# Kernel optimization log

Measured on AMD Instinct MI355X. Metric: run time of the kernel, lower is better.

Reference implementation:

```python
import jax, jax.numpy as jnp
import numpy as np

B, N, A, O = 16, 128, 32, 64
VD, QD, H = 768, 768, 1024


def setup_inputs() -> dict:
    key = jax.random.key(0)
    ks = jax.random.split(key, 10)
    inp = {
        "q": jax.random.normal(ks[0], (B, N, 1, QD), dtype=jnp.float32),
        "att1": jax.random.uniform(ks[1], (B, N, A, O), dtype=jnp.float32),
        "obj_reps": jax.random.normal(ks[2], (B, O, VD), dtype=jnp.float32),
        "tags_attention": jax.random.randint(ks[3], (B, N, A), 0, 2, dtype=jnp.int32),
        "t": 1,
        # FCNet (weight_norm Linear + ReLU) params; dropout is identity at eval
        "vw": jax.random.normal(ks[4], (H, VD), dtype=jnp.float32) * (1.0 / np.sqrt(VD)),
        "vb": jnp.zeros((H,), dtype=jnp.float32),
        "qw": jax.random.normal(ks[5], (H, QD), dtype=jnp.float32) * (1.0 / np.sqrt(QD)),
        "qb": jnp.zeros((H,), dtype=jnp.float32),
        "lw": jax.random.normal(ks[6], (1, H), dtype=jnp.float32) * (1.0 / np.sqrt(H)),
        "lb": jnp.zeros((1,), dtype=jnp.float32),
    }
    return inp


def reference(q, att1, obj_reps, tags_attention, t, vw, vb, qw, qb, lw, lb):
    # v: [b,n,a,d] = att1 [b,n,a,o] contracted with obj_reps [b,o,d]
    v = jnp.einsum('bnao,bod->bnad', att1, obj_reps)
    # FCNet projections (weight_norm linear + ReLU, dropout off at eval)
    v_proj = jax.nn.relu(jnp.einsum('bnad,hd->bnah', v, vw) + vb)      # [b,n,a,h]
    q_proj = jax.nn.relu(jnp.einsum('bnkd,hd->bnkh', q, qw) + qb)      # [b,n,1,h]
    joint = v_proj * q_proj                                            # broadcast over a
    logits = (jnp.einsum('bnah,oh->bnao', joint, lw) + lb)[..., 0]     # [b,n,a]
    logits = logits / jnp.asarray(t, logits.dtype)
    mask = (tags_attention > 0)
    masked_logits = jnp.where(mask, logits, jnp.asarray(-1e30, logits.dtype))
    att2 = jax.nn.softmax(masked_logits, axis=-1)                       # [b,n,a]
    # att2[:,:,None,:] @ att1 -> [b,n,1,o] -> squeeze
    attention_last = jnp.einsum('bna,bnao->bno', att2, att1)
    return attention_last
```

## Files before the change

kernel.cpp:

```cpp
#include <hip/hip_runtime.h>

#define B_ 16
#define N_ 128
#define A_ 32
#define O_ 64
#define VD_ 768
#define H_ 1024

typedef short s16x8 __attribute__((ext_vector_type(8)));
typedef short s16x4 __attribute__((ext_vector_type(4)));
typedef float f32x4 __attribute__((ext_vector_type(4)));

#define MFMA(a, b, c) __builtin_amdgcn_mfma_f32_16x16x32_bf16(a, b, c, 0, 0, 0)

__device__ __forceinline__ short bf_hi(float x) {
    return (short)(__float_as_uint(x) >> 16);
}
__device__ __forceinline__ short bf_lo(float x) {
    float r = x - __uint_as_float(__float_as_uint(x) & 0xffff0000u);
    return (short)(__float_as_uint(r) >> 16);
}

__device__ __forceinline__ void gload16(const void* g, void* l) {
    __builtin_amdgcn_global_load_lds(
        (const __attribute__((address_space(1))) void*)g,
        (__attribute__((address_space(3))) void*)l, 16, 0, 0);
}

__global__ __launch_bounds__(256)
void cvt_split(const float* __restrict__ obj, const float* __restrict__ q,
               const float* __restrict__ vw, const float* __restrict__ qw,
               short* __restrict__ objh, short* __restrict__ objl,
               short* __restrict__ qh, short* __restrict__ ql,
               short* __restrict__ vwh, short* __restrict__ qwh)
{
    const int bid = blockIdx.x;
    const float* src; short* hi; short* lo; int base4;
    if (bid < 192)      { src = obj; hi = objh; lo = objl; base4 = bid * 1024; }
    else if (bid < 576) { src = q;   hi = qh;   lo = ql;   base4 = (bid - 192) * 1024; }
    else if (bid < 768) { src = vw;  hi = vwh;  lo = nullptr; base4 = (bid - 576) * 1024; }
    else                { src = qw;  hi = qwh;  lo = nullptr; base4 = (bid - 768) * 1024; }
    #pragma unroll
    for (int it = 0; it < 4; ++it) {
        const size_t f4 = (size_t)base4 + it * 256 + threadIdx.x;
        const float4 v = *(const float4*)(src + f4 * 4);
        const float ff[4] = {v.x, v.y, v.z, v.w};
        s16x4 h4;
        #pragma unroll
        for (int e = 0; e < 4; ++e) h4[e] = bf_hi(ff[e]);
        *(s16x4*)(hi + f4 * 4) = h4;
        if (lo) {
            s16x4 l4;
            #pragma unroll
            for (int e = 0; e < 4; ++e) l4[e] = bf_lo(ff[e]);
            *(s16x4*)(lo + f4 * 4) = l4;
        }
    }
}

__global__ __launch_bounds__(256)
void gemm_split(const short* __restrict__ objh, const short* __restrict__ objl,
                const short* __restrict__ qh, const short* __restrict__ ql,
                const short* __restrict__ vwh, const short* __restrict__ qwh,
                const float* __restrict__ qb, const float* __restrict__ lwp,
                short* __restrict__ Wth, float* __restrict__ ub)
{
    __shared__ __align__(16) short lds[3 * 4096];
    const int bid = blockIdx.x;
    const bool isA = bid < 256;
    const int lb_ = isA ? bid : bid - 256;
    const int r0 = (lb_ >> 4) * 64;
    const int h0 = (lb_ & 15) * 64;
    const short* Xh = isA ? objh : qh;
    const short* Xl = isA ? objl : ql;
    const short* Bh = isA ? vwh : qwh;

    const int tid = threadIdx.x;
    const int w = tid >> 6, l = tid & 63;
    const int wm = (w >> 1) * 32, wn = (w & 1) * 32;
    const int g = l >> 4, c16 = l & 15;

    const int row0 = tid >> 3, u0 = (tid & 7) ^ (row0 & 7);
    const int unit1 = 256 + tid;
    const int row1 = unit1 >> 3, u1 = (unit1 & 7) ^ (row1 & 7);
    const short* pXh = Xh + (size_t)r0 * VD_;
    const short* pXl = Xl + (size_t)r0 * VD_;
    const short* pBh = Bh + (size_t)h0 * VD_;
    int go0 = row0 * VD_ + u0 * 8;
    int go1 = row1 * VD_ + u1 * 8;
    short* const d0 = &lds[w * 512];

    f32x4 acc[2][2] = {};

    for (int c = 0; c < VD_ / 64; ++c) {
        __syncthreads();
        gload16(pXh + go0, d0);
        gload16(pXh + go1, d0 + 2048);
        gload16(pXl + go0, d0 + 4096);
        gload16(pXl + go1, d0 + 4096 + 2048);
        gload16(pBh + go0, d0 + 8192);
        gload16(pBh + go1, d0 + 8192 + 2048);
        go0 += 64; go1 += 64;
        __syncthreads();
        #pragma unroll
        for (int s = 0; s < 2; ++s) {
            s16x8 ah[2], al[2], bh2[2];
            #pragma unroll
            for (int i = 0; i < 2; ++i) {
                const int m = wm + i * 16 + c16;
                const int us = (((s * 4 + g) ^ (m & 7)) * 8);
                ah[i]  = *(const s16x8*)&lds[m * 64 + us];
                al[i]  = *(const s16x8*)&lds[4096 + m * 64 + us];
                const int n = wn + i * 16 + c16;
                const int vs = (((s * 4 + g) ^ (n & 7)) * 8);
                bh2[i] = *(const s16x8*)&lds[8192 + n * 64 + vs];
            }
            #pragma unroll
            for (int i = 0; i < 2; ++i)
                #pragma unroll
                for (int j = 0; j < 2; ++j) {
                    acc[i][j] = MFMA(ah[i], bh2[j], acc[i][j]);
                    acc[i][j] = MFMA(al[i], bh2[j], acc[i][j]);
                }
        }
    }

    #pragma unroll
    for (int i = 0; i < 2; ++i)
        #pragma unroll
        for (int j = 0; j < 2; ++j) {
            const int h = h0 + wn + j * 16 + c16;
            if (isA) {
                const int o = wm + i * 16 + g * 4;
                s16x4 hi4;
                #pragma unroll
                for (int r = 0; r < 4; ++r) hi4[r] = bf_hi(acc[i][j][r]);
                const size_t dst = ((size_t)(lb_ >> 4) * H_ + h) * O_ + o;
                *(s16x4*)&Wth[dst] = hi4;
            } else {
                const float bv = qb[h], sv = lwp[h];
                #pragma unroll
                for (int r = 0; r < 4; ++r) {
                    const int m = r0 + wm + i * 16 + g * 4 + r;
                    ub[(size_t)m * H_ + h] = fmaxf(acc[i][j][r] + bv, 0.f) * sv;
                }
            }
        }
}

__global__ __launch_bounds__(256, 4)
void fused_logits(const float* __restrict__ att1, const short* __restrict__ Wth,
                  const float* __restrict__ ub, const float* __restrict__ vb,
                  const int* __restrict__ tags, const int* __restrict__ tptr,
                  const float* __restrict__ lbptr, float* __restrict__ out)
{
    __shared__ __align__(16) short Ah[64 * 64];
    __shared__ __align__(16) short Wc[2][4096];
    __shared__ float ut[2][1024];
    __shared__ float vbl[1024];
    __shared__ float lgp[4][64];

    const int blk = blockIdx.x;
    const int b = blk >> 6;
    const int n0 = (blk & 63) * 2;
    const int tid = threadIdx.x;
    const size_t base_row = (size_t)(b * N_ + n0) * A_;

    const int w = tid >> 6, l = tid & 63;
    const int g = l >> 4, c16 = l & 15;

    const int r0l = l >> 3;
    const int cu  = (l & 7) ^ r0l;
    const short* pW = Wth + (size_t)b * (H_ * O_) + w * 1024 + r0l * 64 + cu * 8;
    short* const dW = &Wc[0][w * 1024 + l * 8];

#define STAGEW(BUFOFF, CI) do { \
        const short* ph_ = pW + (size_t)(CI) * 4096; \
        gload16(ph_,       dW + (BUFOFF)); \
        gload16(ph_ + 512, dW + (BUFOFF) + 512); \
    } while (0)

    STAGEW(0, 0);

    {
        const int row = tid >> 2, qq = tid & 3;
        const float* src = att1 + (base_row + row) * O_ + qq * 16;
        #pragma unroll
        for (int uu = 0; uu < 2; ++uu) {
            const float4 f0 = *(const float4*)(src + uu * 8);
            const float4 f1 = *(const float4*)(src + uu * 8 + 4);
            const float ff[8] = {f0.x, f0.y, f0.z, f0.w, f1.x, f1.y, f1.z, f1.w};
            const int us = ((qq * 2 + uu) ^ (row & 7)) * 8;
            s16x8 hi;
            #pragma unroll
            for (int e = 0; e < 8; ++e) hi[e] = bf_hi(ff[e]);
            *(s16x8*)&Ah[row * 64 + us] = hi;
        }
    }

    {
        const float* u0g = ub + (size_t)(b * N_ + n0) * H_;
        const float* u1g = u0g + H_;
        *(float4*)&ut[0][tid * 4] = *(const float4*)(u0g + tid * 4);
        *(float4*)&ut[1][tid * 4] = *(const float4*)(u1g + tid * 4);
        *(float4*)&vbl[tid * 4]   = *(const float4*)(vb + tid * 4);
    }

    __syncthreads();

    s16x8 ahf[4][2];
    #pragma unroll
    for (int i = 0; i < 4; ++i)
        #pragma unroll
        for (int s = 0; s < 2; ++s) {
            const int m = i * 16 + c16;
            const int us = ((s * 4 + g) ^ (m & 7)) * 8;
            ahf[i][s] = *(const s16x8*)&Ah[m * 64 + us];
        }

    const int sr = c16 & 7;
    const int rb = w * 1024 + c16 * 64;
    const int ubo0 = (g ^ sr) * 8;
    const int ubo1 = ((g + 4) ^ sr) * 8;
    const int ulane = w * 16 + c16;

    f32x4 part[4] = {};

    #pragma unroll 2
    for (int t = 0; t < 16; ++t) {
        if (t < 15) {
            STAGEW(((t + 1) & 1) * 4096, t + 1);
            asm volatile("s_waitcnt vmcnt(2)" ::: "memory");
        } else {
            asm volatile("s_waitcnt vmcnt(0)" ::: "memory");
        }
        const int bufo = (t & 1) * 4096;
        const float vbv = vbl[t * 64 + ulane];
        const float uu0 = ut[0][t * 64 + ulane];
        const float uu1 = ut[1][t * 64 + ulane];
        const s16x8 bh0 = *(const s16x8*)&Wc[0][bufo + rb + ubo0];
        const s16x8 bh1 = *(const s16x8*)&Wc[0][bufo + rb + ubo1];
        #pragma unroll
        for (int i = 0; i < 4; ++i) {
            f32x4 acc = {};
            acc = MFMA(ahf[i][0], bh0, acc);
            acc = MFMA(ahf[i][1], bh1, acc);
            const float uu = (i < 2) ? uu0 : uu1;
            #pragma unroll
            for (int r = 0; r < 4; ++r)
                part[i][r] += fmaxf(acc[r] + vbv, 0.f) * uu;
        }
    }
#undef STAGEW

    __syncthreads();

    #pragma unroll
    for (int i = 0; i < 4; ++i)
        #pragma unroll
        for (int r = 0; r < 4; ++r) {
            float v = part[i][r];
            v += __shfl_xor(v, 1, 64);
            v += __shfl_xor(v, 2, 64);
            v += __shfl_xor(v, 4, 64);
            v += __shfl_xor(v, 8, 64);
            if (c16 == 0) lgp[w][i * 16 + g * 4 + r] = v;
        }
    __syncthreads();

    float* sml = &vbl[0];
    if (tid < 64) {
        const float tf = (float)(*tptr);
        const float lsum = lgp[0][tid] + lgp[1][tid] + lgp[2][tid] + lgp[3][tid];
        const float lv = (lsum + *lbptr) / tf;
        const int tg = tags[base_row + tid];
        sml[tid] = (tg > 0) ? lv : -1e30f;
    }
    __syncthreads();

    if (tid < 128) {
        const int nn = tid >> 6, o = tid & 63;
        const float* lr = &sml[nn * 32];
        float m = -3.0e38f;
        #pragma unroll
        for (int a = 0; a < 32; ++a) m = fmaxf(m, lr[a]);
        float s = 0.f, accum = 0.f;
        #pragma unroll
        for (int a = 0; a < 32; ++a) {
            const float e = __expf(lr[a] - m);
            s += e;
            accum += e * att1[(base_row + nn * 32 + a) * O_ + o];
        }
        out[(size_t)(b * N_ + n0 + nn) * O_ + o] = accum / s;
    }
}

extern "C" void kernel_launch(void* const* d_in, const int* in_sizes, int n_in,
                              void* d_out, int out_size, void* d_ws, size_t ws_size,
                              hipStream_t stream)
{
    const float* q    = (const float*)d_in[0];
    const float* att1 = (const float*)d_in[1];
    const float* obj  = (const float*)d_in[2];
    const int*   tags = (const int*)d_in[3];
    const int*   tptr = (const int*)d_in[4];
    const float* vw   = (const float*)d_in[5];
    const float* vb   = (const float*)d_in[6];
    const float* qw   = (const float*)d_in[7];
    const float* qb   = (const float*)d_in[8];
    const float* lw   = (const float*)d_in[9];
    const float* lb   = (const float*)d_in[10];
    float* out = (float*)d_out;

    float* ub   = (float*)d_ws;
    short* Wth  = (short*)(ub + (size_t)B_ * N_ * H_);
    short* objh = Wth + (size_t)B_ * H_ * O_;
    short* objl = objh + (size_t)1024 * VD_;
    short* qh   = objl + (size_t)1024 * VD_;
    short* ql   = qh + (size_t)2048 * VD_;
    short* vwh  = ql + (size_t)2048 * VD_;
    short* qwh  = vwh + (size_t)H_ * VD_;

    cvt_split<<<960, 256, 0, stream>>>(obj, q, vw, qw, objh, objl, qh, ql,
                                       vwh, qwh);
    gemm_split<<<768, 256, 0, stream>>>(objh, objl, qh, ql, vwh, qwh,
                                        qb, lw, Wth, ub);
    fused_logits<<<B_ * 64, 256, 0, stream>>>(att1, Wth, ub, vb, tags,
                                              tptr, lb, out);
}
```

Measured before the change: 48.30 us.

## Double-buffer gemm_split LDS loads and drop low-part split for obj GEMM

Replaces the single-buffered load/compute loop in gemm_split with a two-stage LDS double buffer driven by manual vmcnt waits and raw barriers, so global-to-LDS loads for chunk c+2 overlap MFMA work on chunk c. The obj-side GEMM also stops using the bf16 low-part correction: the objl conversion, its loads and the second MFMA per tile are removed for those blocks. This cuts conversion traffic, load traffic and MFMA count. The cost is lower precision on the Wth path and reliance on hand-counted vmcnt values that must match the number of issued loads per stage.

```diff
diff --git a/kernel.cpp b/kernel.cpp
--- a/kernel.cpp
+++ b/kernel.cpp
@@ -30,14 +30,14 @@
 __global__ __launch_bounds__(256)
 void cvt_split(const float* __restrict__ obj, const float* __restrict__ q,
                const float* __restrict__ vw, const float* __restrict__ qw,
-               short* __restrict__ objh, short* __restrict__ objl,
+               short* __restrict__ objh,
                short* __restrict__ qh, short* __restrict__ ql,
                short* __restrict__ vwh, short* __restrict__ qwh)
 {
     const int bid = blockIdx.x;
     const float* src; short* hi; short* lo; int base4;
-    if (bid < 192)      { src = obj; hi = objh; lo = objl; base4 = bid * 1024; }
-    else if (bid < 576) { src = q;   hi = qh;   lo = ql;   base4 = (bid - 192) * 1024; }
+    if (bid < 192)      { src = obj; hi = objh; lo = nullptr; base4 = bid * 1024; }
+    else if (bid < 576) { src = q;   hi = qh;   lo = ql;      base4 = (bid - 192) * 1024; }
     else if (bid < 768) { src = vw;  hi = vwh;  lo = nullptr; base4 = (bid - 576) * 1024; }
     else                { src = qw;  hi = qwh;  lo = nullptr; base4 = (bid - 768) * 1024; }
     #pragma unroll
@@ -59,20 +59,20 @@
 }
 
 __global__ __launch_bounds__(256)
-void gemm_split(const short* __restrict__ objh, const short* __restrict__ objl,
+void gemm_split(const short* __restrict__ objh,
                 const short* __restrict__ qh, const short* __restrict__ ql,
                 const short* __restrict__ vwh, const short* __restrict__ qwh,
                 const float* __restrict__ qb, const float* __restrict__ lwp,
                 short* __restrict__ Wth, float* __restrict__ ub)
 {
-    __shared__ __align__(16) short lds[3 * 4096];
+    __shared__ __align__(16) short lds[2][3][4096];
     const int bid = blockIdx.x;
     const bool isA = bid < 256;
     const int lb_ = isA ? bid : bid - 256;
     const int r0 = (lb_ >> 4) * 64;
     const int h0 = (lb_ & 15) * 64;
     const short* Xh = isA ? objh : qh;
-    const short* Xl = isA ? objl : ql;
+    const short* Xl = ql;
     const short* Bh = isA ? vwh : qwh;
 
     const int tid = threadIdx.x;
@@ -86,22 +86,40 @@
     const short* pXh = Xh + (size_t)r0 * VD_;
     const short* pXl = Xl + (size_t)r0 * VD_;
     const short* pBh = Bh + (size_t)h0 * VD_;
-    int go0 = row0 * VD_ + u0 * 8;
-    int go1 = row1 * VD_ + u1 * 8;
-    short* const d0 = &lds[w * 512];
+    const int go0 = row0 * VD_ + u0 * 8;
+    const int go1 = row1 * VD_ + u1 * 8;
+    const int wo = w * 512;
+
+#define STAGE(BUF, CI) do { \
+        const int co_ = (CI) * 64; \
+        gload16(pXh + go0 + co_, &lds[BUF][0][wo]); \
+        gload16(pXh + go1 + co_, &lds[BUF][0][wo + 2048]); \
+        if (!isA) { \
+            gload16(pXl + go0 + co_, &lds[BUF][1][wo]); \
+            gload16(pXl + go1 + co_, &lds[BUF][1][wo + 2048]); \
+        } \
+        gload16(pBh + go0 + co_, &lds[BUF][2][wo]); \
+        gload16(pBh + go1 + co_, &lds[BUF][2][wo + 2048]); \
+    } while (0)
+
+    STAGE(0, 0);
+    STAGE(1, 1);
 
     f32x4 acc[2][2] = {};
 
+    #pragma unroll 2
     for (int c = 0; c < VD_ / 64; ++c) {
-        __syncthreads();
-        gload16(pXh + go0, d0);
-        gload16(pXh + go1, d0 + 2048);
-        gload16(pXl + go0, d0 + 4096);
-        gload16(pXl + go1, d0 + 4096 + 2048);
-        gload16(pBh + go0, d0 + 8192);
-        gload16(pBh + go1, d0 + 8192 + 2048);
-        go0 += 64; go1 += 64;
-        __syncthreads();
+        if (c < VD_ / 64 - 1) {
+            if (isA) asm volatile("s_waitcnt vmcnt(4)" ::: "memory");
+            else     asm volatile("s_waitcnt vmcnt(6)" ::: "memory");
+        } else {
+            asm volatile("s_waitcnt vmcnt(0)" ::: "memory");
+        }
+        asm volatile("s_barrier" ::: "memory");
+
+        const short* bXh = &lds[c & 1][0][0];
+        const short* bXl = &lds[c & 1][1][0];
+        const short* bBh = &lds[c & 1][2][0];
         #pragma unroll
         for (int s = 0; s < 2; ++s) {
             s16x8 ah[2], al[2], bh2[2];
@@ -109,21 +127,27 @@
             for (int i = 0; i < 2; ++i) {
                 const int m = wm + i * 16 + c16;
                 const int us = (((s * 4 + g) ^ (m & 7)) * 8);
-                ah[i]  = *(const s16x8*)&lds[m * 64 + us];
-                al[i]  = *(const s16x8*)&lds[4096 + m * 64 + us];
+                ah[i]  = *(const s16x8*)&bXh[m * 64 + us];
+                if (!isA) al[i] = *(const s16x8*)&bXl[m * 64 + us];
                 const int n = wn + i * 16 + c16;
                 const int vs = (((s * 4 + g) ^ (n & 7)) * 8);
-                bh2[i] = *(const s16x8*)&lds[8192 + n * 64 + vs];
+                bh2[i] = *(const s16x8*)&bBh[n * 64 + vs];
             }
             #pragma unroll
             for (int i = 0; i < 2; ++i)
                 #pragma unroll
                 for (int j = 0; j < 2; ++j) {
                     acc[i][j] = MFMA(ah[i], bh2[j], acc[i][j]);
-                    acc[i][j] = MFMA(al[i], bh2[j], acc[i][j]);
+                    if (!isA) acc[i][j] = MFMA(al[i], bh2[j], acc[i][j]);
                 }
         }
-    }
+
+        asm volatile("s_waitcnt lgkmcnt(0)" ::: "memory");
+        __builtin_amdgcn_sched_barrier(0);
+        asm volatile("s_barrier" ::: "memory");
+        if (c + 2 < VD_ / 64) STAGE(c & 1, c + 2);
+    }
+#undef STAGE
 
     #pragma unroll
     for (int i = 0; i < 2; ++i)
@@ -315,15 +339,13 @@
     float* ub   = (float*)d_ws;
     short* Wth  = (short*)(ub + (size_t)B_ * N_ * H_);
     short* objh = Wth + (size_t)B_ * H_ * O_;
-    short* objl = objh + (size_t)1024 * VD_;
-    short* qh   = objl + (size_t)1024 * VD_;
+    short* qh   = objh + (size_t)1024 * VD_;
     short* ql   = qh + (size_t)2048 * VD_;
     short* vwh  = ql + (size_t)2048 * VD_;
     short* qwh  = vwh + (size_t)H_ * VD_;
 
-    cvt_split<<<960, 256, 0, stream>>>(obj, q, vw, qw, objh, objl, qh, ql,
-                                       vwh, qwh);
-    gemm_split<<<768, 256, 0, stream>>>(objh, objl, qh, ql, vwh, qwh,
+    cvt_split<<<960, 256, 0, stream>>>(obj, q, vw, qw, objh, qh, ql, vwh, qwh);
+    gemm_split<<<768, 256, 0, stream>>>(objh, qh, ql, vwh, qwh,
                                         qb, lw, Wth, ub);
     fused_logits<<<B_ * 64, 256, 0, stream>>>(att1, Wth, ub, vb, tags,
                                               tptr, lb, out);
```

Result: faster. 46.29 us (-4.2%).

## Fuse bf16 conversion into GEMM with register-prefetched double-buffered LDS

Applied to the files above, without the earlier changes.

Removes the separate conversion kernel and has the GEMM load fp32 inputs directly, truncate them to bf16 in registers, and write into a double-buffered LDS tile. The next-next chunk is prefetched into registers while the current one is computed. It also drops the hi/lo split on the activations, which halves the MFMA count but lowers the precision of the obj/q projections to plain bf16. One kernel launch and the intermediate bf16 global round-trip go away, at the cost of more register pressure and synchronous global loads inside the loop.

```diff
diff --git a/kernel.cpp b/kernel.cpp
--- a/kernel.cpp
+++ b/kernel.cpp
@@ -16,9 +16,11 @@
 __device__ __forceinline__ short bf_hi(float x) {
     return (short)(__float_as_uint(x) >> 16);
 }
-__device__ __forceinline__ short bf_lo(float x) {
-    float r = x - __uint_as_float(__float_as_uint(x) & 0xffff0000u);
-    return (short)(__float_as_uint(r) >> 16);
+__device__ __forceinline__ void cvthi8(const float4& f0, const float4& f1,
+                                       s16x8& hi) {
+    const float ff[8] = {f0.x, f0.y, f0.z, f0.w, f1.x, f1.y, f1.z, f1.w};
+    #pragma unroll
+    for (int e = 0; e < 8; ++e) hi[e] = bf_hi(ff[e]);
 }
 
 __device__ __forceinline__ void gload16(const void* g, void* l) {
@@ -27,103 +29,93 @@
         (__attribute__((address_space(3))) void*)l, 16, 0, 0);
 }
 
-__global__ __launch_bounds__(256)
-void cvt_split(const float* __restrict__ obj, const float* __restrict__ q,
-               const float* __restrict__ vw, const float* __restrict__ qw,
-               short* __restrict__ objh, short* __restrict__ objl,
-               short* __restrict__ qh, short* __restrict__ ql,
-               short* __restrict__ vwh, short* __restrict__ qwh)
+__global__ __launch_bounds__(256, 3)
+void gemm_cvt(const float* __restrict__ obj, const float* __restrict__ q,
+              const float* __restrict__ vw, const float* __restrict__ qw,
+              const float* __restrict__ qb, const float* __restrict__ lwp,
+              short* __restrict__ Wth, float* __restrict__ ub)
 {
-    const int bid = blockIdx.x;
-    const float* src; short* hi; short* lo; int base4;
-    if (bid < 192)      { src = obj; hi = objh; lo = objl; base4 = bid * 1024; }
-    else if (bid < 576) { src = q;   hi = qh;   lo = ql;   base4 = (bid - 192) * 1024; }
-    else if (bid < 768) { src = vw;  hi = vwh;  lo = nullptr; base4 = (bid - 576) * 1024; }
-    else                { src = qw;  hi = qwh;  lo = nullptr; base4 = (bid - 768) * 1024; }
-    #pragma unroll
-    for (int it = 0; it < 4; ++it) {
-        const size_t f4 = (size_t)base4 + it * 256 + threadIdx.x;
-        const float4 v = *(const float4*)(src + f4 * 4);
-        const float ff[4] = {v.x, v.y, v.z, v.w};
-        s16x4 h4;
-        #pragma unroll
-        for (int e = 0; e < 4; ++e) h4[e] = bf_hi(ff[e]);
-        *(s16x4*)(hi + f4 * 4) = h4;
-        if (lo) {
-            s16x4 l4;
-            #pragma unroll
-            for (int e = 0; e < 4; ++e) l4[e] = bf_lo(ff[e]);
-            *(s16x4*)(lo + f4 * 4) = l4;
-        }
-    }
-}
-
-__global__ __launch_bounds__(256)
-void gemm_split(const short* __restrict__ objh, const short* __restrict__ objl,
-                const short* __restrict__ qh, const short* __restrict__ ql,
-                const short* __restrict__ vwh, const short* __restrict__ qwh,
-                const float* __restrict__ qb, const float* __restrict__ lwp,
-                short* __restrict__ Wth, float* __restrict__ ub)
-{
-    __shared__ __align__(16) short lds[3 * 4096];
+    __shared__ __align__(16) short lds2[2][2][4096];
     const int bid = blockIdx.x;
     const bool isA = bid < 256;
     const int lb_ = isA ? bid : bid - 256;
     const int r0 = (lb_ >> 4) * 64;
     const int h0 = (lb_ & 15) * 64;
-    const short* Xh = isA ? objh : qh;
-    const short* Xl = isA ? objl : ql;
-    const short* Bh = isA ? vwh : qwh;
+    const float* X  = isA ? obj : q;
+    const float* Bm = isA ? vw : qw;
 
     const int tid = threadIdx.x;
     const int w = tid >> 6, l = tid & 63;
     const int wm = (w >> 1) * 32, wn = (w & 1) * 32;
     const int g = l >> 4, c16 = l & 15;
 
-    const int row0 = tid >> 3, u0 = (tid & 7) ^ (row0 & 7);
-    const int unit1 = 256 + tid;
-    const int row1 = unit1 >> 3, u1 = (unit1 & 7) ^ (row1 & 7);
-    const short* pXh = Xh + (size_t)r0 * VD_;
-    const short* pXl = Xl + (size_t)r0 * VD_;
-    const short* pBh = Bh + (size_t)h0 * VD_;
-    int go0 = row0 * VD_ + u0 * 8;
-    int go1 = row1 * VD_ + u1 * 8;
-    short* const d0 = &lds[w * 512];
+    const int srow = tid >> 2, q4 = tid & 3;
+    const float* pX = X  + (size_t)(r0 + srow) * VD_ + q4 * 16;
+    const float* pB = Bm + (size_t)(h0 + srow) * VD_ + q4 * 16;
+    const int u0s = ((q4 * 2) ^ (srow & 7)) * 8;
+    const int u1s = ((q4 * 2 + 1) ^ (srow & 7)) * 8;
+    const int rowb = srow * 64;
+
+    float4 rx0, rx1, rx2, rx3, rb0, rb1, rb2, rb3;
+
+#define LOADREG(CI) do { \
+        const float* px_ = pX + (CI) * 64; \
+        rx0 = *(const float4*)(px_); \
+        rx1 = *(const float4*)(px_ + 4); \
+        rx2 = *(const float4*)(px_ + 8); \
+        rx3 = *(const float4*)(px_ + 12); \
+        const float* pb_ = pB + (CI) * 64; \
+        rb0 = *(const float4*)(pb_); \
+        rb1 = *(const float4*)(pb_ + 4); \
+        rb2 = *(const float4*)(pb_ + 8); \
+        rb3 = *(const float4*)(pb_ + 12); \
+    } while (0)
+
+#define CVTWRITE(BUF) do { \
+        s16x8 hx0_, hx1_, hb0_, hb1_; \
+        cvthi8(rx0, rx1, hx0_); cvthi8(rx2, rx3, hx1_); \
+        cvthi8(rb0, rb1, hb0_); cvthi8(rb2, rb3, hb1_); \
+        *(s16x8*)&lds2[BUF][0][rowb + u0s] = hx0_; \
+        *(s16x8*)&lds2[BUF][0][rowb + u1s] = hx1_; \
+        *(s16x8*)&lds2[BUF][1][rowb + u0s] = hb0_; \
+        *(s16x8*)&lds2[BUF][1][rowb + u1s] = hb1_; \
+    } while (0)
+
+    LOADREG(0);
+    CVTWRITE(0);
+    LOADREG(1);
+    __syncthreads();
 
     f32x4 acc[2][2] = {};
 
+    #pragma unroll 2
     for (int c = 0; c < VD_ / 64; ++c) {
-        __syncthreads();
-        gload16(pXh + go0, d0);
-        gload16(pXh + go1, d0 + 2048);
-        gload16(pXl + go0, d0 + 4096);
-        gload16(pXl + go1, d0 + 4096 + 2048);
-        gload16(pBh + go0, d0 + 8192);
-        gload16(pBh + go1, d0 + 8192 + 2048);
-        go0 += 64; go1 += 64;
-        __syncthreads();
+        const short* bX = &lds2[c & 1][0][0];
+        const short* bB = &lds2[c & 1][1][0];
         #pragma unroll
         for (int s = 0; s < 2; ++s) {
-            s16x8 ah[2], al[2], bh2[2];
+            s16x8 ah[2], bh2[2];
             #pragma unroll
             for (int i = 0; i < 2; ++i) {
                 const int m = wm + i * 16 + c16;
                 const int us = (((s * 4 + g) ^ (m & 7)) * 8);
-                ah[i]  = *(const s16x8*)&lds[m * 64 + us];
-                al[i]  = *(const s16x8*)&lds[4096 + m * 64 + us];
+                ah[i]  = *(const s16x8*)&bX[m * 64 + us];
                 const int n = wn + i * 16 + c16;
                 const int vs = (((s * 4 + g) ^ (n & 7)) * 8);
-                bh2[i] = *(const s16x8*)&lds[8192 + n * 64 + vs];
+                bh2[i] = *(const s16x8*)&bB[n * 64 + vs];
             }
             #pragma unroll
             for (int i = 0; i < 2; ++i)
                 #pragma unroll
-                for (int j = 0; j < 2; ++j) {
+                for (int j = 0; j < 2; ++j)
                     acc[i][j] = MFMA(ah[i], bh2[j], acc[i][j]);
-                    acc[i][j] = MFMA(al[i], bh2[j], acc[i][j]);
-                }
-        }
-    }
+        }
+        if (c < VD_ / 64 - 1) CVTWRITE((c + 1) & 1);
+        if (c < VD_ / 64 - 2) LOADREG(c + 2);
+        if (c < VD_ / 64 - 1) __syncthreads();
+    }
+#undef LOADREG
+#undef CVTWRITE
 
     #pragma unroll
     for (int i = 0; i < 2; ++i)
@@ -189,11 +181,9 @@
         for (int uu = 0; uu < 2; ++uu) {
             const float4 f0 = *(const float4*)(src + uu * 8);
             const float4 f1 = *(const float4*)(src + uu * 8 + 4);
-            const float ff[8] = {f0.x, f0.y, f0.z, f0.w, f1.x, f1.y, f1.z, f1.w};
             const int us = ((qq * 2 + uu) ^ (row & 7)) * 8;
             s16x8 hi;
-            #pragma unroll
-            for (int e = 0; e < 8; ++e) hi[e] = bf_hi(ff[e]);
+            cvthi8(f0, f1, hi);
             *(s16x8*)&Ah[row * 64 + us] = hi;
         }
     }
@@ -312,19 +302,10 @@
     const float* lb   = (const float*)d_in[10];
     float* out = (float*)d_out;
 
-    float* ub   = (float*)d_ws;
-    short* Wth  = (short*)(ub + (size_t)B_ * N_ * H_);
-    short* objh = Wth + (size_t)B_ * H_ * O_;
-    short* objl = objh + (size_t)1024 * VD_;
-    short* qh   = objl + (size_t)1024 * VD_;
-    short* ql   = qh + (size_t)2048 * VD_;
-    short* vwh  = ql + (size_t)2048 * VD_;
-    short* qwh  = vwh + (size_t)H_ * VD_;
-
-    cvt_split<<<960, 256, 0, stream>>>(obj, q, vw, qw, objh, objl, qh, ql,
-                                       vwh, qwh);
-    gemm_split<<<768, 256, 0, stream>>>(objh, objl, qh, ql, vwh, qwh,
-                                        qb, lw, Wth, ub);
+    float* ub  = (float*)d_ws;
+    short* Wth = (short*)(ub + (size_t)B_ * N_ * H_);
+
+    gemm_cvt<<<768, 256, 0, stream>>>(obj, q, vw, qw, qb, lw, Wth, ub);
     fused_logits<<<B_ * 64, 256, 0, stream>>>(att1, Wth, ub, vb, tags,
                                               tptr, lb, out);
 }
```

After: 56.20 us. 1.16x slower.
